# Kernel optimization log

Hardware: AMD Instinct MI355X
Metric: run time of the kernel (lower is better)

The kernel has to match this reference:

```python
import jax, jax.numpy as jnp
import numpy as np


def setup_inputs() -> dict:
    key = jax.random.key(0)
    k1, k2, k3 = jax.random.split(key, 3)
    B, C, H, W = 32, 192, 64, 64
    L = 64  # number of unique quantization levels in the sos codebook
    x = jax.random.normal(k1, (B, C, H, W), dtype=jnp.float32) * 4.0
    means = jax.random.normal(k2, (B, C, H, W), dtype=jnp.float32)
    # sorted 1-D codebook of unique quantizer levels (sos.unique_values)
    codebook = jnp.sort(jax.random.normal(k3, (L,), dtype=jnp.float32) * 4.0)
    return {"x": x, "means": means, "codebook": codebook}


def _nearest_level(r, codebook):
    """Vectorized version of transform_map: for each element of r, the index of
    the nearest codebook value (argmin |codebook - r|), using searchsorted on
    the sorted codebook instead of a dense [N, L] distance matrix."""
    L = codebook.shape[0]
    pos = jnp.clip(jnp.searchsorted(codebook, r), 1, L - 1)  # right neighbor
    left = codebook[pos - 1]
    right = codebook[pos]
    return jnp.where(r - left <= right - r, pos - 1, pos)  # int32 symbols


def reference(x, means, codebook):
    # quantize(mode='symbols'): subtract means, map each value to the index of
    # the nearest codebook level (the map_sos_cdf dict lookup / argmin loop).
    r = x - means
    symbols = _nearest_level(r, codebook)          # [B,C,H,W] int32
    # dequantize: map symbols back to float levels (map_cdf_sos) and add means.
    y_hat = jnp.take(codebook, symbols) + means    # [B,C,H,W] float32
    return symbols, y_hat
```

## Files before the change

kernel.cpp:

```cpp
#include <hip/hip_runtime.h>
#include <math.h>


__global__ __launch_bounds__(256) void quant_dequant_kernel(
    const float4* __restrict__ x4,
    const float4* __restrict__ m4,
    const float*  __restrict__ codebook,
    float4* __restrict__ sym_out,
    float4* __restrict__ yhat_out,
    int n4)
{
    __shared__ float s_cb[64];
    __shared__ float s_mid[64];

    const int tid = threadIdx.x;
    if (tid < 64) s_cb[tid] = codebook[tid];
    __syncthreads();
    if (tid < 64)
        s_mid[tid] = (tid < 63) ? 0.5f * (s_cb[tid] + s_cb[tid + 1])
                                : INFINITY;
    __syncthreads();

    const int i = blockIdx.x * blockDim.x + tid;
    if (i >= n4) return;

    const float4 xv = x4[i];
    const float4 mv = m4[i];

    float r[4] = { xv.x - mv.x, xv.y - mv.y, xv.z - mv.z, xv.w - mv.w };
    float mm[4] = { mv.x, mv.y, mv.z, mv.w };
    float sym[4], yh[4];

#pragma unroll
    for (int k = 0; k < 4; ++k) {
        int pos = 0;
#pragma unroll
        for (int s = 32; s > 0; s >>= 1) {
            pos += (s_mid[pos + s - 1] < r[k]) ? s : 0;
        }
        sym[k] = (float)pos;
        yh[k]  = s_cb[pos] + mm[k];
    }

    sym_out[i]  = make_float4(sym[0], sym[1], sym[2], sym[3]);
    yhat_out[i] = make_float4(yh[0], yh[1], yh[2], yh[3]);
}

extern "C" void kernel_launch(void* const* d_in, const int* in_sizes, int n_in,
                              void* d_out, int out_size, void* d_ws, size_t ws_size,
                              hipStream_t stream)
{
    const float* x     = (const float*)d_in[0];
    const float* means = (const float*)d_in[1];
    const float* cb    = (const float*)d_in[2];

    const int n  = in_sizes[0];
    const int n4 = n / 4;

    float* out = (float*)d_out;

    const int block = 256;
    const int grid  = (n4 + block - 1) / block;

    quant_dequant_kernel<<<grid, block, 0, stream>>>(
        (const float4*)x, (const float4*)means, cb,
        (float4*)out, (float4*)(out + n), n4);
}
```

Baseline: 333.0 us.

## Replace binary search with LUT bucket lookup and grid-stride persistent loop

Each block builds a 1024-cell lookup table mapping uniform value buckets to a starting codebook index, then does a short linear walk over midpoints instead of a 6-step binary search in shared memory. The launch becomes a fixed grid of 2048 blocks with a 4-way unrolled grid-stride loop, and stores become nontemporal. This is meant to cut shared-memory lookups and raise memory-level parallelism on a bandwidth-bound kernel. In exchange every block pays for building the table, and the linear walk has data-dependent divergence.

```diff
diff --git a/kernel.cpp b/kernel.cpp
--- a/kernel.cpp
+++ b/kernel.cpp
@@ -1,17 +1,29 @@
 #include <hip/hip_runtime.h>
 #include <math.h>
 
+
+#define NCELL 1024
+
+typedef float f32x4 __attribute__((ext_vector_type(4)));
+
+__device__ __forceinline__ int cellof(float v, float lo, float scale) {
+    float t = (v - lo) * scale;
+    t = fminf(fmaxf(t, 0.0f), (float)(NCELL - 1));
+    return (int)t;
+}
 
 __global__ __launch_bounds__(256) void quant_dequant_kernel(
     const float4* __restrict__ x4,
     const float4* __restrict__ m4,
     const float*  __restrict__ codebook,
-    float4* __restrict__ sym_out,
-    float4* __restrict__ yhat_out,
+    f32x4* __restrict__ sym_out,
+    f32x4* __restrict__ yhat_out,
     int n4)
 {
     __shared__ float s_cb[64];
     __shared__ float s_mid[64];
+    __shared__ unsigned short s_fm[64];
+    __shared__ unsigned short s_lut[NCELL];
 
     const int tid = threadIdx.x;
     if (tid < 64) s_cb[tid] = codebook[tid];
@@ -19,31 +31,74 @@
     if (tid < 64)
         s_mid[tid] = (tid < 63) ? 0.5f * (s_cb[tid] + s_cb[tid + 1])
                                 : INFINITY;
+    const float lo    = s_cb[0];
+    const float hi    = s_cb[63];
+    const float range = hi - lo;
+    const float scale = (range > 0.0f) ? ((float)NCELL / range) : 0.0f;
+    __syncthreads();
+    if (tid < 64)
+        s_fm[tid] = (tid < 63) ? (unsigned short)cellof(s_mid[tid], lo, scale)
+                               : (unsigned short)0xFFFF;
     __syncthreads();
 
-    const int i = blockIdx.x * blockDim.x + tid;
-    if (i >= n4) return;
-
-    const float4 xv = x4[i];
-    const float4 mv = m4[i];
-
-    float r[4] = { xv.x - mv.x, xv.y - mv.y, xv.z - mv.z, xv.w - mv.w };
-    float mm[4] = { mv.x, mv.y, mv.z, mv.w };
-    float sym[4], yh[4];
-
 #pragma unroll
-    for (int k = 0; k < 4; ++k) {
+    for (int e = 0; e < NCELL / 256; ++e) {
+        const int c = tid + e * 256;
         int pos = 0;
 #pragma unroll
-        for (int s = 32; s > 0; s >>= 1) {
-            pos += (s_mid[pos + s - 1] < r[k]) ? s : 0;
+        for (int s = 32; s > 0; s >>= 1)
+            pos += (s_fm[pos + s - 1] < c) ? s : 0;
+        s_lut[c] = (unsigned short)pos;
+    }
+    __syncthreads();
+
+    const int stride = gridDim.x * blockDim.x;
+    int i = blockIdx.x * blockDim.x + tid;
+
+    for (; i + 3 * stride < n4; i += 4 * stride) {
+        float4 xv[4], mv[4];
+#pragma unroll
+        for (int u = 0; u < 4; ++u) {
+            xv[u] = x4[i + u * stride];
+            mv[u] = m4[i + u * stride];
         }
-        sym[k] = (float)pos;
-        yh[k]  = s_cb[pos] + mm[k];
+#pragma unroll
+        for (int u = 0; u < 4; ++u) {
+            float rr[4] = { xv[u].x - mv[u].x, xv[u].y - mv[u].y,
+                            xv[u].z - mv[u].z, xv[u].w - mv[u].w };
+            float mm[4] = { mv[u].x, mv[u].y, mv[u].z, mv[u].w };
+            f32x4 sy, yh;
+#pragma unroll
+            for (int k = 0; k < 4; ++k) {
+                const float r = rr[k];
+                const int idx = cellof(r, lo, scale);
+                int pos = (int)s_lut[idx];
+                while (s_mid[pos] < r) ++pos;
+                sy[k] = (float)pos;
+                yh[k] = s_cb[pos] + mm[k];
+            }
+            __builtin_nontemporal_store(sy, &sym_out[i + u * stride]);
+            __builtin_nontemporal_store(yh, &yhat_out[i + u * stride]);
+        }
     }
-
-    sym_out[i]  = make_float4(sym[0], sym[1], sym[2], sym[3]);
-    yhat_out[i] = make_float4(yh[0], yh[1], yh[2], yh[3]);
+    for (; i < n4; i += stride) {
+        const float4 xv = x4[i];
+        const float4 mv = m4[i];
+        float rr[4] = { xv.x - mv.x, xv.y - mv.y, xv.z - mv.z, xv.w - mv.w };
+        float mm[4] = { mv.x, mv.y, mv.z, mv.w };
+        f32x4 sy, yh;
+#pragma unroll
+        for (int k = 0; k < 4; ++k) {
+            const float r = rr[k];
+            const int idx = cellof(r, lo, scale);
+            int pos = (int)s_lut[idx];
+            while (s_mid[pos] < r) ++pos;
+            sy[k] = (float)pos;
+            yh[k] = s_cb[pos] + mm[k];
+        }
+        __builtin_nontemporal_store(sy, &sym_out[i]);
+        __builtin_nontemporal_store(yh, &yhat_out[i]);
+    }
 }
 
 extern "C" void kernel_launch(void* const* d_in, const int* in_sizes, int n_in,
@@ -60,9 +115,9 @@
     float* out = (float*)d_out;
 
     const int block = 256;
-    const int grid  = (n4 + block - 1) / block;
+    const int grid  = 2048;
 
     quant_dequant_kernel<<<grid, block, 0, stream>>>(
         (const float4*)x, (const float4*)means, cb,
-        (float4*)out, (float4*)(out + n), n4);
+        (f32x4*)out, (f32x4*)(out + n), n4);
 }
```

After: 353.5 us. 6.2% more time.

## Replace per-element binary search with precomputed uniform-cell LUT lookup

Applied to the files above, without the earlier changes.

Adds a one-block kernel that builds a 1024-cell uniform grid over the codebook range, storing for each cell the first midpoint index and how many midpoints fall in it. The main kernel loads this table into shared memory and resolves each value with one cell lookup plus a comparison, with a short scan only for crowded cells, instead of a 6-step dependent binary search over shared memory. Each thread now handles two float4s so the global loads are issued before the table setup. The cost is an extra kernel launch, 8KB of shared memory loaded per block, and data-dependent loops where cells hold several midpoints.

```diff
diff --git a/kernel.cpp b/kernel.cpp
--- a/kernel.cpp
+++ b/kernel.cpp
@@ -1,49 +1,137 @@
 #include <hip/hip_runtime.h>
 #include <math.h>
 
+
+#define NCELL 1024
+
+__device__ __forceinline__ int cellof(float v, float lo, float scale) {
+    float t = (v - lo) * scale;
+    t = fminf(fmaxf(t, 0.0f), (float)(NCELL - 1));
+    return (int)t;
+}
+
+__global__ __launch_bounds__(256) void build_lut_kernel(
+    const float* __restrict__ codebook,
+    float* __restrict__ ws_mid,
+    float* __restrict__ ws_emid,
+    unsigned int* __restrict__ ws_epos)
+{
+    __shared__ float s_cb[64];
+    __shared__ float s_mid[64];
+    __shared__ unsigned short s_fm[64];
+
+    const int tid = threadIdx.x;
+    if (tid < 64) s_cb[tid] = codebook[tid];
+    __syncthreads();
+    const float lo    = s_cb[0];
+    const float range = s_cb[63] - lo;
+    const float scale = (range > 0.0f) ? ((float)NCELL / range) : 0.0f;
+    if (tid < 64) {
+        float mid = (tid < 63) ? 0.5f * (s_cb[tid] + s_cb[tid + 1]) : INFINITY;
+        s_mid[tid]  = mid;
+        ws_mid[tid] = mid;
+        s_fm[tid] = (tid < 63) ? (unsigned short)cellof(mid, lo, scale)
+                               : (unsigned short)0xFFFF;
+    }
+    __syncthreads();
+
+#pragma unroll
+    for (int e = 0; e < NCELL / 256; ++e) {
+        const int c = tid + e * 256;
+        int pos = 0;
+#pragma unroll
+        for (int s = 32; s > 0; s >>= 1)
+            pos += (s_fm[pos + s - 1] < c) ? s : 0;
+        int pos1 = 0;
+#pragma unroll
+        for (int s = 32; s > 0; s >>= 1)
+            pos1 += (s_fm[pos1 + s - 1] < c + 1) ? s : 0;
+        const int n = pos1 - pos;
+        ws_emid[c] = (n > 0) ? s_mid[pos] : INFINITY;
+        ws_epos[c] = (unsigned int)pos | ((unsigned int)n << 16);
+    }
+}
 
 __global__ __launch_bounds__(256) void quant_dequant_kernel(
     const float4* __restrict__ x4,
     const float4* __restrict__ m4,
     const float*  __restrict__ codebook,
+    const float*  __restrict__ ws_mid,
+    const float4* __restrict__ ws_emid4,
+    const uint4*  __restrict__ ws_epos4,
     float4* __restrict__ sym_out,
     float4* __restrict__ yhat_out,
     int n4)
 {
-    __shared__ float s_cb[64];
-    __shared__ float s_mid[64];
+    __shared__ float        s_emid[NCELL];
+    __shared__ unsigned int s_epos[NCELL];
+    __shared__ float        s_cb[64];
+    __shared__ float        s_mid[64];
 
     const int tid = threadIdx.x;
-    if (tid < 64) s_cb[tid] = codebook[tid];
-    __syncthreads();
-    if (tid < 64)
-        s_mid[tid] = (tid < 63) ? 0.5f * (s_cb[tid] + s_cb[tid + 1])
-                                : INFINITY;
+
+    const float4 ev  = ws_emid4[tid];
+    const uint4  pv  = ws_epos4[tid];
+    const float  cbv  = (tid < 64) ? codebook[tid] : 0.0f;
+    const float  midv = (tid < 64) ? ws_mid[tid]   : 0.0f;
+
+    const int base = blockIdx.x * 512 + tid;
+    const bool full = (blockIdx.x * 512 + 512) <= n4;
+    float4 xa, xb, ma, mb;
+    if (full) {
+        xa = x4[base];       ma = m4[base];
+        xb = x4[base + 256]; mb = m4[base + 256];
+    } else {
+        if (base < n4)       { xa = x4[base];       ma = m4[base]; }
+        if (base + 256 < n4) { xb = x4[base + 256]; mb = m4[base + 256]; }
+    }
+
+    ((float4*)s_emid)[tid] = ev;
+    ((uint4*)s_epos)[tid]  = pv;
+    if (tid < 64) { s_cb[tid] = cbv; s_mid[tid] = midv; }
     __syncthreads();
 
-    const int i = blockIdx.x * blockDim.x + tid;
-    if (i >= n4) return;
+    const float lo    = s_cb[0];
+    const float range = s_cb[63] - lo;
+    const float scale = (range > 0.0f) ? ((float)NCELL / range) : 0.0f;
 
-    const float4 xv = x4[i];
-    const float4 mv = m4[i];
-
-    float r[4] = { xv.x - mv.x, xv.y - mv.y, xv.z - mv.z, xv.w - mv.w };
-    float mm[4] = { mv.x, mv.y, mv.z, mv.w };
-    float sym[4], yh[4];
+    float xr[8] = { xa.x, xa.y, xa.z, xa.w, xb.x, xb.y, xb.z, xb.w };
+    float mr[8] = { ma.x, ma.y, ma.z, ma.w, mb.x, mb.y, mb.z, mb.w };
+    float sv[8], yv[8];
 
 #pragma unroll
-    for (int k = 0; k < 4; ++k) {
-        int pos = 0;
-#pragma unroll
-        for (int s = 32; s > 0; s >>= 1) {
-            pos += (s_mid[pos + s - 1] < r[k]) ? s : 0;
+    for (int k = 0; k < 8; ++k) {
+        const float m = mr[k];
+        const float r = xr[k] - m;
+        const int   c = cellof(r, lo, scale);
+        const float        emid = s_emid[c];
+        const unsigned int ep   = s_epos[c];
+        const int pos0 = (int)(ep & 0xFFFFu);
+        const int n    = (int)(ep >> 16);
+        int pos = pos0 + ((emid < r) ? 1 : 0);
+        if (n > 1) {
+            for (int j = 1; j < n; ++j)
+                pos += (s_mid[pos0 + j] < r) ? 1 : 0;
         }
-        sym[k] = (float)pos;
-        yh[k]  = s_cb[pos] + mm[k];
+        sv[k] = (float)pos;
+        yv[k] = s_cb[pos] + m;
     }
 
-    sym_out[i]  = make_float4(sym[0], sym[1], sym[2], sym[3]);
-    yhat_out[i] = make_float4(yh[0], yh[1], yh[2], yh[3]);
+    if (full) {
+        sym_out[base]         = make_float4(sv[0], sv[1], sv[2], sv[3]);
+        yhat_out[base]        = make_float4(yv[0], yv[1], yv[2], yv[3]);
+        sym_out[base + 256]   = make_float4(sv[4], sv[5], sv[6], sv[7]);
+        yhat_out[base + 256]  = make_float4(yv[4], yv[5], yv[6], yv[7]);
+    } else {
+        if (base < n4) {
+            sym_out[base]  = make_float4(sv[0], sv[1], sv[2], sv[3]);
+            yhat_out[base] = make_float4(yv[0], yv[1], yv[2], yv[3]);
+        }
+        if (base + 256 < n4) {
+            sym_out[base + 256]  = make_float4(sv[4], sv[5], sv[6], sv[7]);
+            yhat_out[base + 256] = make_float4(yv[4], yv[5], yv[6], yv[7]);
+        }
+    }
 }
 
 extern "C" void kernel_launch(void* const* d_in, const int* in_sizes, int n_in,
@@ -59,10 +147,16 @@
 
     float* out = (float*)d_out;
 
+    float*        ws_mid  = (float*)d_ws;
+    float*        ws_emid = (float*)((char*)d_ws + 256);
+    unsigned int* ws_epos = (unsigned int*)((char*)d_ws + 256 + 4096);
+
+    build_lut_kernel<<<1, 256, 0, stream>>>(cb, ws_mid, ws_emid, ws_epos);
+
     const int block = 256;
-    const int grid  = (n4 + block - 1) / block;
-
+    const int grid  = (n4 + 511) / 512;
     quant_dequant_kernel<<<grid, block, 0, stream>>>(
         (const float4*)x, (const float4*)means, cb,
+        ws_mid, (const float4*)ws_emid, (const uint4*)ws_epos,
         (float4*)out, (float4*)(out + n), n4);
 }
```

Measured after the change: 335.8 us. About the same (+0.8%).
